# Kernel tuning notes

Measured on AMD Instinct MI355X. Metric: run time of the kernel, lower is better.

The kernel has to match this reference:

```python
import jax, jax.numpy as jnp
import numpy as np

THRESH = 0.1

def _ternary_ste(w):
    # STE: forward = ternary(w), backward = identity
    wq = jnp.where(w > THRESH, 1.0, jnp.where(w < -THRESH, -1.0, 0.0))
    return w + jax.lax.stop_gradient(wq - w)

def _act_quant_ste(x):
    # training-mode ActivationQuantizer: scale = 127/max|x| (buffer update, detached)
    scale = jax.lax.stop_gradient(127.0 / jnp.max(jnp.abs(x)))
    xq = jnp.clip(jnp.round(x * scale), -128.0, 127.0) / scale
    return x + jax.lax.stop_gradient(xq - x)

def setup_inputs() -> dict:
    key = jax.random.key(0)
    k1, k2, k3, k4, k5 = jax.random.split(key, 5)
    B, D_IN, D_H, D_OUT = 8192, 784, 4096, 10
    x = jax.random.normal(k1, (B, D_IN), dtype=jnp.float32)
    w1 = jax.random.normal(k2, (D_H, D_IN), dtype=jnp.float32) * 0.05
    b1 = jax.random.normal(k3, (D_H,), dtype=jnp.float32) * 0.01
    w2 = jax.random.normal(k4, (D_OUT, D_H), dtype=jnp.float32) * 0.05
    b2 = jax.random.normal(k5, (D_OUT,), dtype=jnp.float32) * 0.01
    return {"x": x, "w1": w1, "b1": b1, "w2": w2, "b2": b2}

def reference(x, w1, b1, w2, b2):
    x = x.reshape(-1, 784)
    h = x @ _ternary_ste(w1).T + b1          # [B, D_H]
    h = jax.nn.relu(h)
    h = _act_quant_ste(h)
    logits = h @ _ternary_ste(w2).T + b2     # [B, D_OUT]
    return jax.nn.log_softmax(logits, axis=1)
```

## Files before the change

### kernel.cpp

```cpp
#include <hip/hip_runtime.h>

#define M_B   8192
#define K_IN  784
#define KPAD  832
#define N_H   4096
#define N_OUT 10
#define BM    256
#define BN    128
#define BK    64

typedef __attribute__((ext_vector_type(8))) short bf16x8;
typedef __attribute__((ext_vector_type(4))) float f32x4;
typedef unsigned short u16;
typedef unsigned int   u32;

__device__ __forceinline__ u16 f2bf(float f) {
    union { float f; u32 u; } v; v.f = f;
    u32 r = (v.u + 0x7fffu + ((v.u >> 16) & 1u)) >> 16;
    return (u16)r;
}
__device__ __forceinline__ float bf2f(u16 h) {
    union { u32 u; float f; } v; v.u = ((u32)h) << 16;
    return v.f;
}
__device__ __forceinline__ void load_lds16(const void* g, void* l) {
    __builtin_amdgcn_global_load_lds(
        (const __attribute__((address_space(1))) void*)g,
        (__attribute__((address_space(3))) void*)l, 16, 0, 0);
}
__device__ __forceinline__ float sb(int w, int i) {
    return (float)((w << (24 - 8 * i)) >> 24);
}

__global__ void prep_all(const float* __restrict__ x, const float* __restrict__ w1,
                         const float* __restrict__ w2,
                         u16* __restrict__ xb, u16* __restrict__ w1b,
                         signed char* __restrict__ w2c, u32* __restrict__ maxb) {
    const int blk = blockIdx.x;
    const int tid = threadIdx.x;
    if (blk < 3328) {
        int idx = blk * 256 + tid;
        int row = idx / 104;
        int col = (idx - row * 104) * 8;
        u16 v[8];
        if (col < K_IN) {
            const float4* p = (const float4*)(x + (size_t)row * K_IN + col);
            float4 a = p[0], b = p[1];
            v[0] = f2bf(a.x); v[1] = f2bf(a.y); v[2] = f2bf(a.z); v[3] = f2bf(a.w);
            v[4] = f2bf(b.x); v[5] = f2bf(b.y); v[6] = f2bf(b.z); v[7] = f2bf(b.w);
        } else {
            #pragma unroll
            for (int i = 0; i < 8; ++i) v[i] = 0;
        }
        *(uint4*)(xb + (size_t)row * KPAD + col) = *(const uint4*)v;
    } else if (blk < 4992) {
        int idx = (blk - 3328) * 256 + tid;
        int row = idx / 104;
        int col = (idx - row * 104) * 8;
        u16 v[8];
        if (col < K_IN) {
            const float4* p = (const float4*)(w1 + (size_t)row * K_IN + col);
            float4 a = p[0], b = p[1];
            float ff[8] = {a.x, a.y, a.z, a.w, b.x, b.y, b.z, b.w};
            #pragma unroll
            for (int i = 0; i < 8; ++i)
                v[i] = ff[i] > 0.1f ? 0x3F80u : (ff[i] < -0.1f ? 0xBF80u : 0u);
        } else {
            #pragma unroll
            for (int i = 0; i < 8; ++i) v[i] = 0;
        }
        *(uint4*)(w1b + (size_t)row * KPAD + col) = *(const uint4*)v;
    } else {
        int k = (blk - 4992) * 256 + tid;
        if (k == 0) *maxb = 0u;
        if (k >= N_H) return;
        signed char v[16];
        #pragma unroll
        for (int o = 0; o < 16; ++o) v[o] = 0;
        #pragma unroll
        for (int o = 0; o < N_OUT; ++o) {
            float f = w2[(size_t)o * N_H + k];
            v[o] = f > 0.1f ? 1 : (f < -0.1f ? -1 : 0);
        }
        *(int4*)(w2c + (size_t)k * 16) = *(const int4*)v;
    }
}

__global__ __launch_bounds__(256, 2) void gemm1(
    const u16* __restrict__ A,
    const u16* __restrict__ Bw,
    const float* __restrict__ b1,
    u16* __restrict__ Ht,
    u32* __restrict__ maxb)
{
    __shared__ __align__(16) u16 As[BM * BK];
    __shared__ __align__(16) u16 Bs[BN * BK];
    __shared__ float wmax[4];

    const int tid  = threadIdx.x;
    const int lane = tid & 63;
    const int wave = tid >> 6;
    const int wr = wave >> 1, wc = wave & 1;
    const int bm = blockIdx.x, bn = blockIdx.y;

    f32x4 acc[8][4] = {};

    const u16* ga[8]; u16* la[8];
    #pragma unroll
    for (int j = 0; j < 8; ++j) {
        int s = tid + 256 * j;
        int grow = s >> 3;
        int gcol = (((s & 7) ^ ((s >> 3) & 7)) << 3);
        ga[j] = A + (size_t)(bm * BM + grow) * KPAD + gcol;
        la[j] = &As[s * 8];
    }
    const u16* gb[4]; u16* lb[4];
    #pragma unroll
    for (int j = 0; j < 4; ++j) {
        int s = tid + 256 * j;
        int grow = s >> 3;
        int gcol = (((s & 7) ^ ((s >> 3) & 7)) << 3);
        gb[j] = Bw + (size_t)(bn * BN + grow) * KPAD + gcol;
        lb[j] = &Bs[s * 8];
    }

    const int rA = (wr * 128 + (lane & 15)) * BK;
    const int rB = (wc * 64  + (lane & 15)) * BK;
    const int c0 = (((lane >> 4) ^ (lane & 7)) << 3);

    for (int t = 0; t < 13; ++t) {
        #pragma unroll
        for (int j = 0; j < 8; ++j) { load_lds16(ga[j], la[j]); ga[j] += BK; }
        #pragma unroll
        for (int j = 0; j < 4; ++j) { load_lds16(gb[j], lb[j]); gb[j] += BK; }
        __syncthreads();

        #pragma unroll
        for (int h = 0; h < 2; ++h) {
            const int ch = c0 ^ (h << 5);
            bf16x8 af[8], bfr[4];
            #pragma unroll
            for (int i = 0; i < 8; ++i) af[i]  = *(const bf16x8*)&As[rA + i * 16 * BK + ch];
            #pragma unroll
            for (int j = 0; j < 4; ++j) bfr[j] = *(const bf16x8*)&Bs[rB + j * 16 * BK + ch];
            #pragma unroll
            for (int i = 0; i < 8; ++i)
                #pragma unroll
                for (int j = 0; j < 4; ++j)
                    acc[i][j] = __builtin_amdgcn_mfma_f32_16x16x32_bf16(
                        af[i], bfr[j], acc[i][j], 0, 0, 0);
        }
        __syncthreads();
    }

    const int colb = bn * BN + wc * 64 + (lane & 15);
    const int rowb = bm * BM + wr * 128 + ((lane >> 4) << 2);

    float lmax = 0.f;
    #pragma unroll
    for (int j = 0; j < 4; ++j) {
        const int col = colb + j * 16;
        const float bias = b1[col];
        u16* hp = Ht + (size_t)col * M_B + rowb;
        #pragma unroll
        for (int i = 0; i < 8; ++i) {
            u32 pk[2];
            #pragma unroll
            for (int h = 0; h < 2; ++h) {
                float v0 = fmaxf(acc[i][j][2 * h]     + bias, 0.f);
                float v1 = fmaxf(acc[i][j][2 * h + 1] + bias, 0.f);
                lmax = fmaxf(lmax, fmaxf(v0, v1));
                pk[h] = (u32)f2bf(v0) | ((u32)f2bf(v1) << 16);
            }
            *(uint2*)(hp + i * 16) = make_uint2(pk[0], pk[1]);
        }
    }
    #pragma unroll
    for (int s = 32; s; s >>= 1) lmax = fmaxf(lmax, __shfl_down(lmax, s, 64));
    if (lane == 0) wmax[wave] = lmax;
    __syncthreads();
    if (tid == 0)
        atomicMax(maxb, __float_as_uint(
            fmaxf(fmaxf(wmax[0], wmax[1]), fmaxf(wmax[2], wmax[3]))));
}

__global__ __launch_bounds__(256) void gemm2_part(
    const u16* __restrict__ Ht,
    const signed char* __restrict__ W2c,
    const u32* __restrict__ maxb,
    float* __restrict__ part)
{
    __shared__ int4 sW[128];
    const int tid = threadIdx.x;
    const int bx = blockIdx.x;
    const int ky = blockIdx.y;
    if (tid < 128) sW[tid] = *(const int4*)(W2c + (size_t)(ky * 128 + tid) * 16);
    const float scale = 127.0f / __uint_as_float(*maxb);
    __syncthreads();

    const int b0 = bx * 512 + tid * 2;
    float s0[N_OUT] = {}, s1[N_OUT] = {};
    const u16* hp = Ht + (size_t)(ky * 128) * M_B + b0;

    #pragma unroll 8
    for (int kk = 0; kk < 128; ++kk) {
        const int4 wv = sW[kk];
        float w[N_OUT];
        w[0] = sb(wv.x, 0); w[1] = sb(wv.x, 1); w[2] = sb(wv.x, 2); w[3] = sb(wv.x, 3);
        w[4] = sb(wv.y, 0); w[5] = sb(wv.y, 1); w[6] = sb(wv.y, 2); w[7] = sb(wv.y, 3);
        w[8] = sb(wv.z, 0); w[9] = sb(wv.z, 1);
        const u32 hv = *(const u32*)hp;
        hp += M_B;
        const float q0 = fminf(rintf(bf2f((u16)(hv & 0xffffu)) * scale), 127.0f);
        const float q1 = fminf(rintf(bf2f((u16)(hv >> 16))     * scale), 127.0f);
        #pragma unroll
        for (int o = 0; o < N_OUT; ++o) {
            s0[o] = fmaf(q0, w[o], s0[o]);
            s1[o] = fmaf(q1, w[o], s1[o]);
        }
    }
    float* p = part + ((size_t)ky * M_B + b0) * N_OUT;
    #pragma unroll
    for (int o = 0; o < N_OUT; ++o) { p[o] = s0[o]; p[N_OUT + o] = s1[o]; }
}

__global__ __launch_bounds__(256) void lsm_out(
    const float* __restrict__ part,
    const float* __restrict__ b2,
    const u32* __restrict__ maxb,
    float* __restrict__ out)
{
    __shared__ float red[8][32][N_OUT];
    const int tid = threadIdx.x;
    const int g = tid >> 5;
    const int r = tid & 31;
    const int b = blockIdx.x * 32 + r;

    float s[N_OUT] = {};
    #pragma unroll
    for (int i = 0; i < 4; ++i) {
        const float* pp = part + ((size_t)(g * 4 + i) * M_B + b) * N_OUT;
        #pragma unroll
        for (int o = 0; o < N_OUT; ++o) s[o] += pp[o];
    }
    #pragma unroll
    for (int o = 0; o < N_OUT; ++o) red[g][r][o] = s[o];
    __syncthreads();

    if (tid < 32) {
        const float invs = __uint_as_float(*maxb) / 127.0f;
        float v[N_OUT];
        #pragma unroll
        for (int o = 0; o < N_OUT; ++o) v[o] = red[0][tid][o];
        #pragma unroll
        for (int g2 = 1; g2 < 8; ++g2)
            #pragma unroll
            for (int o = 0; o < N_OUT; ++o) v[o] += red[g2][tid][o];

        float lg[N_OUT], mx = -1e30f;
        #pragma unroll
        for (int o = 0; o < N_OUT; ++o) {
            lg[o] = fmaf(v[o], invs, b2[o]);
            mx = fmaxf(mx, lg[o]);
        }
        float se = 0.f;
        #pragma unroll
        for (int o = 0; o < N_OUT; ++o) se += expf(lg[o] - mx);
        const float lse = logf(se) + mx;
        float* op = out + (size_t)(blockIdx.x * 32 + tid) * N_OUT;
        #pragma unroll
        for (int o = 0; o < N_OUT; ++o) op[o] = lg[o] - lse;
    }
}

extern "C" void kernel_launch(void* const* d_in, const int* in_sizes, int n_in,
                              void* d_out, int out_size, void* d_ws, size_t ws_size,
                              hipStream_t stream) {
    const float* x  = (const float*)d_in[0];
    const float* w1 = (const float*)d_in[1];
    const float* b1 = (const float*)d_in[2];
    const float* w2 = (const float*)d_in[3];
    const float* b2 = (const float*)d_in[4];
    float* out = (float*)d_out;

    char* ws = (char*)d_ws;
    u16* xb  = (u16*)(ws);
    float* part = (float*)(ws);
    u16* w1b = (u16*)(ws + 13631488);
    u16* ht  = (u16*)(ws + 20447232);
    signed char* w2c = (signed char*)(ws + 87556096);
    u32* maxb = (u32*)(ws + 87621632);

    prep_all<<<5008, 256, 0, stream>>>(x, w1, w2, xb, w1b, w2c, maxb);
    gemm1<<<dim3(32, 32), 256, 0, stream>>>(xb, w1b, b1, ht, maxb);
    gemm2_part<<<dim3(16, 32), 256, 0, stream>>>(ht, w2c, maxb, part);
    lsm_out<<<256, 256, 0, stream>>>(part, b2, maxb, out);
}
```

Before: 172.4 us.

## Shrink gemm1 M-tile and restructure gemm2 K-split with in-block wave reduction

gemm1 now uses 128x128 tiles instead of 256x128, which doubles the grid to 2048 blocks and raises the occupancy hint to 3 blocks per CU. This is meant to fill the 256 CUs better and cut accumulator register pressure, at the cost of less data reuse per tile. gemm2_part now splits K into 8 chunks of 512 and has its four waves interleave over K, reducing their results through LDS before writing. This leaves 8 partial slices instead of 32, which shrinks the partial-sum traffic, and lsm_out now sums only those 8 slices.

```diff
diff --git a/kernel.cpp b/kernel.cpp
--- a/kernel.cpp
+++ b/kernel.cpp
@@ -5,7 +5,7 @@
 #define KPAD  832
 #define N_H   4096
 #define N_OUT 10
-#define BM    256
+#define BM    128
 #define BN    128
 #define BK    64
 
@@ -86,7 +86,7 @@
     }
 }
 
-__global__ __launch_bounds__(256, 2) void gemm1(
+__global__ __launch_bounds__(256, 3) void gemm1(
     const u16* __restrict__ A,
     const u16* __restrict__ Bw,
     const float* __restrict__ b1,
@@ -103,11 +103,11 @@
     const int wr = wave >> 1, wc = wave & 1;
     const int bm = blockIdx.x, bn = blockIdx.y;
 
-    f32x4 acc[8][4] = {};
-
-    const u16* ga[8]; u16* la[8];
-    #pragma unroll
-    for (int j = 0; j < 8; ++j) {
+    f32x4 acc[4][4] = {};
+
+    const u16* ga[4]; u16* la[4];
+    #pragma unroll
+    for (int j = 0; j < 4; ++j) {
         int s = tid + 256 * j;
         int grow = s >> 3;
         int gcol = (((s & 7) ^ ((s >> 3) & 7)) << 3);
@@ -124,13 +124,13 @@
         lb[j] = &Bs[s * 8];
     }
 
-    const int rA = (wr * 128 + (lane & 15)) * BK;
-    const int rB = (wc * 64  + (lane & 15)) * BK;
+    const int rA = (wr * 64 + (lane & 15)) * BK;
+    const int rB = (wc * 64 + (lane & 15)) * BK;
     const int c0 = (((lane >> 4) ^ (lane & 7)) << 3);
 
     for (int t = 0; t < 13; ++t) {
         #pragma unroll
-        for (int j = 0; j < 8; ++j) { load_lds16(ga[j], la[j]); ga[j] += BK; }
+        for (int j = 0; j < 4; ++j) { load_lds16(ga[j], la[j]); ga[j] += BK; }
         #pragma unroll
         for (int j = 0; j < 4; ++j) { load_lds16(gb[j], lb[j]); gb[j] += BK; }
         __syncthreads();
@@ -138,13 +138,13 @@
         #pragma unroll
         for (int h = 0; h < 2; ++h) {
             const int ch = c0 ^ (h << 5);
-            bf16x8 af[8], bfr[4];
-            #pragma unroll
-            for (int i = 0; i < 8; ++i) af[i]  = *(const bf16x8*)&As[rA + i * 16 * BK + ch];
+            bf16x8 af[4], bfr[4];
+            #pragma unroll
+            for (int i = 0; i < 4; ++i) af[i]  = *(const bf16x8*)&As[rA + i * 16 * BK + ch];
             #pragma unroll
             for (int j = 0; j < 4; ++j) bfr[j] = *(const bf16x8*)&Bs[rB + j * 16 * BK + ch];
             #pragma unroll
-            for (int i = 0; i < 8; ++i)
+            for (int i = 0; i < 4; ++i)
                 #pragma unroll
                 for (int j = 0; j < 4; ++j)
                     acc[i][j] = __builtin_amdgcn_mfma_f32_16x16x32_bf16(
@@ -154,7 +154,7 @@
     }
 
     const int colb = bn * BN + wc * 64 + (lane & 15);
-    const int rowb = bm * BM + wr * 128 + ((lane >> 4) << 2);
+    const int rowb = bm * BM + wr * 64 + ((lane >> 4) << 2);
 
     float lmax = 0.f;
     #pragma unroll
@@ -163,7 +163,7 @@
         const float bias = b1[col];
         u16* hp = Ht + (size_t)col * M_B + rowb;
         #pragma unroll
-        for (int i = 0; i < 8; ++i) {
+        for (int i = 0; i < 4; ++i) {
             u32 pk[2];
             #pragma unroll
             for (int h = 0; h < 2; ++h) {
@@ -190,27 +190,32 @@
     const u32* __restrict__ maxb,
     float* __restrict__ part)
 {
-    __shared__ int4 sW[128];
-    const int tid = threadIdx.x;
+    __shared__ int4 sW[512];
+    __shared__ float red[4][128][N_OUT];
+    const int tid  = threadIdx.x;
+    const int lane = tid & 63;
+    const int wave = tid >> 6;
     const int bx = blockIdx.x;
     const int ky = blockIdx.y;
-    if (tid < 128) sW[tid] = *(const int4*)(W2c + (size_t)(ky * 128 + tid) * 16);
+
+    sW[tid]       = *(const int4*)(W2c + (size_t)(ky * 512 + tid) * 16);
+    sW[tid + 256] = *(const int4*)(W2c + (size_t)(ky * 512 + tid + 256) * 16);
     const float scale = 127.0f / __uint_as_float(*maxb);
     __syncthreads();
 
-    const int b0 = bx * 512 + tid * 2;
+    const int b0 = bx * 128 + lane * 2;
     float s0[N_OUT] = {}, s1[N_OUT] = {};
-    const u16* hp = Ht + (size_t)(ky * 128) * M_B + b0;
+    const u16* hp = Ht + (size_t)(ky * 512 + wave) * M_B + b0;
 
     #pragma unroll 8
-    for (int kk = 0; kk < 128; ++kk) {
-        const int4 wv = sW[kk];
+    for (int it = 0; it < 128; ++it) {
+        const int4 wv = sW[it * 4 + wave];
         float w[N_OUT];
         w[0] = sb(wv.x, 0); w[1] = sb(wv.x, 1); w[2] = sb(wv.x, 2); w[3] = sb(wv.x, 3);
         w[4] = sb(wv.y, 0); w[5] = sb(wv.y, 1); w[6] = sb(wv.y, 2); w[7] = sb(wv.y, 3);
         w[8] = sb(wv.z, 0); w[9] = sb(wv.z, 1);
         const u32 hv = *(const u32*)hp;
-        hp += M_B;
+        hp += 4 * M_B;
         const float q0 = fminf(rintf(bf2f((u16)(hv & 0xffffu)) * scale), 127.0f);
         const float q1 = fminf(rintf(bf2f((u16)(hv >> 16))     * scale), 127.0f);
         #pragma unroll
@@ -219,9 +224,19 @@
             s1[o] = fmaf(q1, w[o], s1[o]);
         }
     }
-    float* p = part + ((size_t)ky * M_B + b0) * N_OUT;
-    #pragma unroll
-    for (int o = 0; o < N_OUT; ++o) { p[o] = s0[o]; p[N_OUT + o] = s1[o]; }
+    #pragma unroll
+    for (int o = 0; o < N_OUT; ++o) {
+        red[wave][lane * 2][o]     = s0[o];
+        red[wave][lane * 2 + 1][o] = s1[o];
+    }
+    __syncthreads();
+
+    if (tid < 128) {
+        float* p = part + ((size_t)ky * M_B + bx * 128 + tid) * N_OUT;
+        #pragma unroll
+        for (int o = 0; o < N_OUT; ++o)
+            p[o] = red[0][tid][o] + red[1][tid][o] + red[2][tid][o] + red[3][tid][o];
+    }
 }
 
 __global__ __launch_bounds__(256) void lsm_out(
@@ -236,15 +251,9 @@
     const int r = tid & 31;
     const int b = blockIdx.x * 32 + r;
 
-    float s[N_OUT] = {};
-    #pragma unroll
-    for (int i = 0; i < 4; ++i) {
-        const float* pp = part + ((size_t)(g * 4 + i) * M_B + b) * N_OUT;
-        #pragma unroll
-        for (int o = 0; o < N_OUT; ++o) s[o] += pp[o];
-    }
-    #pragma unroll
-    for (int o = 0; o < N_OUT; ++o) red[g][r][o] = s[o];
+    const float* pp = part + ((size_t)g * M_B + b) * N_OUT;
+    #pragma unroll
+    for (int o = 0; o < N_OUT; ++o) red[g][r][o] = pp[o];
     __syncthreads();
 
     if (tid < 32) {
@@ -292,7 +301,7 @@
     u32* maxb = (u32*)(ws + 87621632);
 
     prep_all<<<5008, 256, 0, stream>>>(x, w1, w2, xb, w1b, w2c, maxb);
-    gemm1<<<dim3(32, 32), 256, 0, stream>>>(xb, w1b, b1, ht, maxb);
-    gemm2_part<<<dim3(16, 32), 256, 0, stream>>>(ht, w2c, maxb, part);
+    gemm1<<<dim3(64, 32), 256, 0, stream>>>(xb, w1b, b1, ht, maxb);
+    gemm2_part<<<dim3(64, 8), 256, 0, stream>>>(ht, w2c, maxb, part);
     lsm_out<<<256, 256, 0, stream>>>(part, b2, maxb, out);
 }
```

Result: faster. 166.7 us (-3.3%).
